# Kernel optimization log

Hardware: AMD Instinct MI355X
Metric: run time of the kernel (lower is better)

The kernel has to match this reference:

```python
import jax, jax.numpy as jnp
import numpy as np

BN_EPS = 1e-5


def conv3x3(x, w, b):
    # x: [B,C,H,W], w: [O,C,3,3], same padding, stride 1
    y = jax.lax.conv_general_dilated(x, w, (1, 1), ((1, 1), (1, 1)),
                                     dimension_numbers=('NCHW', 'OIHW', 'NCHW'))
    return y + b[None, :, None, None]


def bilinear_sample(x, py, px):
    # x: [B,C,H,W]; py/px: [B,K,H,W] fractional sample coords (zero outside borders)
    B, C, H, W = x.shape
    y0 = jnp.floor(py)
    x0 = jnp.floor(px)
    wy1 = py - y0  # frac weights
    wx1 = px - x0

    def corner(yc, xc, wgt):
        valid = (yc >= 0) & (yc <= H - 1) & (xc >= 0) & (xc <= W - 1)
        yi = jnp.clip(yc, 0, H - 1).astype(jnp.int32)
        xi = jnp.clip(xc, 0, W - 1).astype(jnp.int32)
        # gather per batch: [C,H,W] indexed by [K,H,W] -> [C,K,H,W]
        g = jax.vmap(lambda img, yy, xx: img[:, yy, xx])(x, yi, xi)  # [B,C,K,H,W]
        return g * jnp.where(valid, wgt, 0.0)[:, None]

    return (corner(y0, x0, (1 - wy1) * (1 - wx1))
            + corner(y0, x0 + 1, (1 - wy1) * wx1)
            + corner(y0 + 1, x0, wy1 * (1 - wx1))
            + corner(y0 + 1, x0 + 1, wy1 * wx1))  # [B,C,9,H,W]


def deform_conv(x, conv_w, off_w, off_b, mask_w, mask_b, gamma, beta):
    B, C, H, W = x.shape
    O = conv_w.shape[0]
    offset = conv3x3(x, off_w, off_b)                      # [B,18,H,W]
    mask = jax.nn.sigmoid(conv3x3(x, mask_w, mask_b))      # [B,9,H,W]
    off = offset.reshape(B, 9, 2, H, W)                    # tap k = kh*3+kw, (dy,dx)
    ky = jnp.repeat(jnp.arange(3), 3).astype(x.dtype)      # kernel row per tap
    kx = jnp.tile(jnp.arange(3), 3).astype(x.dtype)        # kernel col per tap
    gy = jnp.arange(H, dtype=x.dtype)
    gx = jnp.arange(W, dtype=x.dtype)
    # sample position = out pos - pad + kernel idx + learned offset
    py = off[:, :, 0] + gy[None, None, :, None] + (ky - 1.0)[None, :, None, None]
    px = off[:, :, 1] + gx[None, None, None, :] + (kx - 1.0)[None, :, None, None]
    val = bilinear_sample(x, py, px)                       # [B,C,9,H,W]
    val = val * mask[:, None]                              # modulated (DCNv2)
    out = jnp.einsum('bckhw,ock->bohw', val, conv_w.reshape(O, C, 9))
    # BatchNorm (training-mode batch stats) + ReLU
    mean = out.mean(axis=(0, 2, 3))
    var = out.var(axis=(0, 2, 3))
    out = (out - mean[None, :, None, None]) * jax.lax.rsqrt(var + BN_EPS)[None, :, None, None]
    out = out * gamma[None, :, None, None] + beta[None, :, None, None]
    return jax.nn.relu(out)


def setup_inputs() -> dict:
    key = jax.random.key(0)
    ks = jax.random.split(key, 8)
    B, Cin, Cout, H, W = 2, 64, 64, 128, 128
    x = jax.random.normal(ks[0], (B, Cin, H, W), dtype=jnp.float32)
    fan = Cin * 9
    conv_w = jax.random.normal(ks[1], (Cout, Cin, 3, 3), dtype=jnp.float32) / np.sqrt(fan)
    # offset/mask convs: small random weights so offsets are non-degenerate but modest
    off_w = jax.random.normal(ks[2], (18, Cin, 3, 3), dtype=jnp.float32) * 0.01
    off_b = jax.random.normal(ks[3], (18,), dtype=jnp.float32) * 0.1
    mask_w = jax.random.normal(ks[4], (9, Cin, 3, 3), dtype=jnp.float32) * 0.01
    mask_b = jnp.zeros((9,), dtype=jnp.float32)
    gamma = jnp.ones((Cout,), dtype=jnp.float32)
    beta = jnp.zeros((Cout,), dtype=jnp.float32)
    return {"x": x, "conv_w": conv_w, "off_w": off_w, "off_b": off_b,
            "mask_w": mask_w, "mask_b": mask_b, "gamma": gamma, "beta": beta}


def reference(x, conv_w, off_w, off_b, mask_w, mask_b, gamma, beta):
    return deform_conv(x, conv_w, off_w, off_b, mask_w, mask_b, gamma, beta)
```

## Files before the change

kernel.cpp:

```cpp
#include <hip/hip_runtime.h>
#include <hip/hip_fp16.h>

typedef __attribute__((ext_vector_type(8))) _Float16 f16x8;
typedef __attribute__((ext_vector_type(4))) float f32x4;
typedef __attribute__((ext_vector_type(4))) unsigned int u32x4;
typedef unsigned int  u32;
typedef unsigned short u16;

constexpr int B_  = 2;
constexpr int C_  = 64;
constexpr int O_  = 64;
constexpr int H_  = 128;
constexpr int W_  = 128;
constexpr int HW_ = H_ * W_;
constexpr int NPIX_ = B_ * HW_;
constexpr float BN_EPS_ = 1e-5f;

constexpr int WCOLS_ = 38;
constexpr int WPIX_  = 7 * WCOLS_;

__device__ __forceinline__ u16 f2bf(float f) {
    u32 u = __float_as_uint(f);
    u = (u + 0x7fffu + ((u >> 16) & 1u)) >> 16;
    return (u16)u;
}
__device__ __forceinline__ float bflo(u32 u) { return __uint_as_float(u << 16); }
__device__ __forceinline__ float bfhi(u32 u) { return __uint_as_float(u & 0xffff0000u); }
__device__ __forceinline__ u16 f2h(float f) { return __half_as_ushort(__float2half(f)); }

__device__ __forceinline__ u32 swz(u32 wpx, u32 seg) {
    return wpx * 64u + ((seg ^ (wpx & 7u)) * 8u);
}

__global__ __launch_bounds__(256)
void prep_kernel(const float* __restrict__ x, const float* __restrict__ conv_w,
                 const float* __restrict__ off_w, const float* __restrict__ mask_w,
                 u16* __restrict__ xt, u16* __restrict__ WpF, u16* __restrict__ W27F) {
    int bid = blockIdx.x, tid = threadIdx.x;
    if (bid < 512) {
        __shared__ u16 tile[64][66];
        int b = bid >> 8;
        int hw0 = (bid & 255) * 64;
        int c = tid >> 2, pq = (tid & 3) * 16;
        const float* src = x + (((size_t)(b * 64 + c)) << 14) + hw0 + pq;
#pragma unroll
        for (int i = 0; i < 4; i++) {
            float4 v = *(const float4*)(src + i * 4);
            tile[pq + i * 4 + 0][c] = f2h(v.x);
            tile[pq + i * 4 + 1][c] = f2h(v.y);
            tile[pq + i * 4 + 2][c] = f2h(v.z);
            tile[pq + i * 4 + 3][c] = f2h(v.w);
        }
        __syncthreads();
        int p = tid >> 2, cs = (tid & 3) * 16;
        uint4* dst = (uint4*)(xt + (((size_t)(b << 14)) + hw0 + p) * 64 + cs);
        dst[0] = *(const uint4*)&tile[p][cs];
        dst[1] = *(const uint4*)&tile[p][cs + 8];
    } else if (bid < 512 + 144) {
        int i = (bid - 512) * 256 + tid;
        int j = i & 7, lane = (i >> 3) & 63, t = (i >> 9) & 3, s = i >> 11;
        int o = t * 16 + (lane & 15);
        int kk = s * 32 + (lane >> 4) * 8 + j;
        int tap = kk >> 6, c = kk & 63;
        WpF[i] = f2h(conv_w[(o * 64 + c) * 9 + tap]);
    } else {
        int i = (bid - 656) * 256 + tid;
        int j = i & 7, lane = (i >> 3) & 63, t = (i >> 9) & 1, s = i >> 10;
        int row = t * 16 + (lane & 15);
        int kk = s * 32 + (lane >> 4) * 8 + j;
        int tap = kk >> 6, c = kk & 63;
        float v = 0.f;
        if (row < 18) v = off_w[(row * 64 + c) * 9 + tap];
        else if (row < 27) v = mask_w[((row - 18) * 64 + c) * 9 + tap];
        W27F[i] = f2h(v);
    }
}

__device__ __forceinline__ void metaBrt(const float* __restrict__ moff,
                                        const float* __restrict__ mmask,
                                        int tap, int p32, int h, int w, int cb,
                                        u32 quad, u32* qc, u32* cwp) {
    float dy = moff[(2 * tap) * 32 + p32];
    float dx = moff[(2 * tap + 1) * 32 + p32];
    float m  = mmask[tap * 32 + p32];
    float kdy = (float)(tap / 3 - 1), kdx = (float)(tap % 3 - 1);
    float py = dy + (float)h + kdy;
    float px = dx + (float)w + kdx;
    float y0 = floorf(py), x0 = floorf(px);
    float ly = py - y0, lx = px - x0, hy = 1.f - ly, hx = 1.f - lx;
    float y1 = y0 + 1.f, x1 = x0 + 1.f;
    bool vy0 = (y0 >= 0.f) && (y0 <= 127.f);
    bool vy1 = (y1 >= 0.f) && (y1 <= 127.f);
    bool vx0 = (x0 >= 0.f) && (x0 <= 127.f);
    bool vx1 = (x1 >= 0.f) && (x1 <= 127.f);
    int iy0 = (int)fminf(fmaxf(y0, 0.f), 127.f);
    int iy1 = (int)fminf(fmaxf(y1, 0.f), 127.f);
    int ix0 = (int)fminf(fmaxf(x0, 0.f), 127.f);
    int ix1 = (int)fminf(fmaxf(x1, 0.f), 127.f);
    int w00 = min(max(iy0 * WCOLS_ + ix0 - cb, 0), WPIX_ - 1);
    int w01 = min(max(iy0 * WCOLS_ + ix1 - cb, 0), WPIX_ - 1);
    int w10 = min(max(iy1 * WCOLS_ + ix0 - cb, 0), WPIX_ - 1);
    int w11 = min(max(iy1 * WCOLS_ + ix1 - cb, 0), WPIX_ - 1);
    qc[0] = swz((u32)w00, quad);
    qc[1] = swz((u32)w01, quad);
    qc[2] = swz((u32)w10, quad);
    qc[3] = swz((u32)w11, quad);
    __half2 c0 = __float2half2_rn((vy0 && vx0) ? hy * hx * m : 0.f);
    __half2 c1 = __float2half2_rn((vy0 && vx1) ? hy * lx * m : 0.f);
    __half2 c2 = __float2half2_rn((vy1 && vx0) ? ly * hx * m : 0.f);
    __half2 c3 = __float2half2_rn((vy1 && vx1) ? ly * lx * m : 0.f);
    cwp[0] = *(const u32*)&c0; cwp[1] = *(const u32*)&c1;
    cwp[2] = *(const u32*)&c2; cwp[3] = *(const u32*)&c3;
}

__device__ __forceinline__ void ld4x(const u16* __restrict__ win, const u32* qc,
                                     u32 sx, uint4* p) {
#pragma unroll
    for (int i = 0; i < 4; i++) p[i] = *(const uint4*)(win + (qc[i] ^ sx));
}

__device__ __forceinline__ f16x8 cmbH(const uint4* p, const u32* cwp) {
    const u32* a = &p[0].x; const u32* b = &p[1].x;
    const u32* c = &p[2].x; const u32* d = &p[3].x;
    __half2 cw0 = *(const __half2*)&cwp[0], cw1 = *(const __half2*)&cwp[1];
    __half2 cw2 = *(const __half2*)&cwp[2], cw3 = *(const __half2*)&cwp[3];
    u32x4 r;
#pragma unroll
    for (int i = 0; i < 4; i++) {
        __half2 t = __hmul2(*(const __half2*)&a[i], cw0);
        t = __hfma2(*(const __half2*)&b[i], cw1, t);
        t = __hfma2(*(const __half2*)&c[i], cw2, t);
        t = __hfma2(*(const __half2*)&d[i], cw3, t);
        r[i] = *(const u32*)&t;
    }
    return __builtin_bit_cast(f16x8, r);
}

template<int TAP>
__device__ __forceinline__ void tapB(const u16* __restrict__ win,
                                     const float* __restrict__ moff,
                                     const float* __restrict__ mmask,
                                     const u16* __restrict__ WpFo,
                                     int p32, int h, int w, int cb, u32 quad,
                                     int lane, uint4 (&pA)[4], u32 (&q)[4],
                                     u32 (&cw)[4], f32x4 (&acc)[2]) {
    uint4 pB[4];
    ld4x(win, q, 32, pB);
    u32 qn[4]; u32 wn[4]; uint4 pC[4];
    if constexpr (TAP < 8) {
        metaBrt(moff, mmask, TAP + 1, p32, h, w, cb, quad, qn, wn);
        ld4x(win, qn, 0, pC);
    }
    f16x8 sv = cmbH(pA, cw);
#pragma unroll
    for (int t = 0; t < 2; t++) {
        f16x8 af = *(const f16x8*)(WpFo + (u32)(2 * TAP) * 2048u + (u32)t * 512u + (u32)lane * 8u);
        acc[t] = __builtin_amdgcn_mfma_f32_16x16x32_f16(af, sv, acc[t], 0, 0, 0);
    }
    sv = cmbH(pB, cw);
#pragma unroll
    for (int t = 0; t < 2; t++) {
        f16x8 af = *(const f16x8*)(WpFo + (u32)(2 * TAP + 1) * 2048u + (u32)t * 512u + (u32)lane * 8u);
        acc[t] = __builtin_amdgcn_mfma_f32_16x16x32_f16(af, sv, acc[t], 0, 0, 0);
    }
    if constexpr (TAP < 8)
        tapB<TAP + 1>(win, moff, mmask, WpFo, p32, h, w, cb, quad, lane, pC, qn, wn, acc);
}

__global__ __launch_bounds__(256, 4)
void gemm_ab_kernel(const u16* __restrict__ xt, const u16* __restrict__ W27F,
                    const u16* __restrict__ WpF,
                    const float* __restrict__ off_b, const float* __restrict__ mask_b,
                    u16* __restrict__ pre16, float* __restrict__ part) {
    __shared__ __align__(16) u16 win[(WPIX_ + 1) * 64];
    __shared__ float moff[18 * 32];
    __shared__ float mmask[9 * 32];
    const int tid = threadIdx.x;
    const int lane = tid & 63, wv = tid >> 6;
    const int pxg = wv & 1, oh = wv >> 1;
    const u32 quad = (u32)(lane >> 4);
    const int r = lane & 15;
    const int pbase = blockIdx.x * 32;
    const int b = pbase >> 14, hwb = pbase & (HW_ - 1);
    const int h = hwb >> 7, w0 = hwb & (W_ - 1);
    const int p32 = pxg * 16 + r;
    const int hw = hwb + p32, w = w0 + p32;
    const int cb = (h - 3) * WCOLS_ + (w0 - 3);
    const u32 bb = (u32)b << 14;

#pragma unroll
    for (int it = 0; it < 9; it++) {
        int i = tid + it * 256;
        if (i < WPIX_ * 8) {
            u32 px = (u32)i >> 3, seg = (u32)i & 7u;
            int wr = (int)px / WCOLS_, wc = (int)px - wr * WCOLS_;
            int row = min(max(h - 3 + wr, 0), H_ - 1);
            int col = min(max(w0 - 3 + wc, 0), W_ - 1);
            u32 g = (bb + (u32)(row * W_ + col)) * 64u + seg * 8u;
            *(uint4*)(&win[swz(px, seg)]) = *(const uint4*)(xt + g);
        } else if (i < WPIX_ * 8 + 8) {
            u32 seg = (u32)(i - WPIX_ * 8);
            *(uint4*)(&win[swz((u32)WPIX_, seg)]) = make_uint4(0, 0, 0, 0);
        }
    }
    __syncthreads();

    {
        u32 aq[9];
#pragma unroll
        for (int tap = 0; tap < 9; tap++) {
            int dh = tap / 3 - 1, dw = tap % 3 - 1;
            int hh = h + dh, ww = w + dw;
            bool valid = (hh >= 0) && (hh < H_) && (ww >= 0) && (ww < W_);
            u32 wpx = valid ? (u32)((3 + dh) * WCOLS_ + (p32 + 3 + dw)) : (u32)WPIX_;
            aq[tap] = swz(wpx, quad);
        }
        const u16* W27Fo = W27F + (u32)oh * 512u;
        f32x4 accA = (f32x4){0.f, 0.f, 0.f, 0.f};
        f16x8 ab[3];
        ab[0] = *(const f16x8*)(win + aq[0]);
        ab[1] = *(const f16x8*)(win + (aq[0] ^ 32u));
        ab[2] = *(const f16x8*)(win + aq[1]);
#pragma unroll
        for (int s = 0; s < 18; s++) {
            f16x8 sv = ab[s % 3];
            if (s + 3 < 18)
                ab[s % 3] = *(const f16x8*)(win + (aq[(s + 3) >> 1] ^ (u32)(((s + 3) & 1) * 32)));
            f16x8 af = *(const f16x8*)(W27Fo + (u32)s * 1024u + (u32)lane * 8u);
            accA = __builtin_amdgcn_mfma_f32_16x16x32_f16(af, sv, accA, 0, 0, 0);
        }
#pragma unroll
        for (int g = 0; g < 4; g++) {
            int o = oh * 16 + (int)quad * 4 + g;
            float v = accA[g];
            if (o < 18) {
                moff[o * 32 + p32] = v + off_b[o];
            } else if (o < 27) {
                v += mask_b[o - 18];
                mmask[(o - 18) * 32 + p32] = 1.f / (1.f + __expf(-v));
            }
        }
    }
    __syncthreads();

    f32x4 acc[2];
    acc[0] = (f32x4){0.f, 0.f, 0.f, 0.f};
    acc[1] = (f32x4){0.f, 0.f, 0.f, 0.f};
    {
        const u16* WpFo = WpF + (u32)oh * 1024u;
        u32 q[4]; u32 cw[4];
        metaBrt(moff, mmask, 0, p32, h, w, cb, quad, q, cw);
        uint4 pA[4];
        ld4x(win, q, 0, pA);
        tapB<0>(win, moff, mmask, WpFo, p32, h, w, cb, quad, lane, pA, q, cw, acc);
    }

    const u32 slot = (u32)(blockIdx.x * 2 + pxg);
#pragma unroll
    for (int t = 0; t < 2; t++) {
#pragma unroll
        for (int g = 0; g < 4; g++) {
            float v = acc[t][g];
            int o = oh * 32 + t * 16 + (int)quad * 4 + g;
            pre16[(u32)(b * 64 + o) * HW_ + hw] = f2bf(v);
            float s = v, s2 = v * v;
#pragma unroll
            for (int off = 8; off >= 1; off >>= 1) {
                s  += __shfl_down(s, off, 16);
                s2 += __shfl_down(s2, off, 16);
            }
            if (r == 0) {
                part[(u32)o * 2048 + slot] = s;
                part[131072 + (u32)o * 2048 + slot] = s2;
            }
        }
    }
}

__global__ __launch_bounds__(256)
void stats_red_kernel(const float* __restrict__ part, float* __restrict__ stats) {
    __shared__ float p4[4];
    int i = blockIdx.x;
    const float* src = part + (u32)(i >> 6) * 131072 + (u32)(i & 63) * 2048;
    float s = 0.f;
    for (int rr = threadIdx.x; rr < 2048; rr += 256) s += src[rr];
#pragma unroll
    for (int off = 32; off >= 1; off >>= 1) s += __shfl_down(s, off);
    if ((threadIdx.x & 63) == 0) p4[threadIdx.x >> 6] = s;
    __syncthreads();
    if (threadIdx.x == 0) stats[i] = p4[0] + p4[1] + p4[2] + p4[3];
}

__global__ __launch_bounds__(256)
void bn_relu_kernel(const u16* __restrict__ pre16, const float* __restrict__ stats,
                    const float* __restrict__ gamma, const float* __restrict__ beta,
                    float* __restrict__ out) {
    int i4 = blockIdx.x * 256 + threadIdx.x;
    int ch = (i4 >> 12) & (O_ - 1);
    float mean = stats[ch] * (1.f / NPIX_);
    float var  = stats[64 + ch] * (1.f / NPIX_) - mean * mean;
    float scale = gamma[ch] * rsqrtf(var + BN_EPS_);
    float shift = beta[ch] - mean * scale;
    uint2 v = ((const uint2*)pre16)[i4];
    float4 o;
    o.x = fmaxf(fmaf(bflo(v.x), scale, shift), 0.f);
    o.y = fmaxf(fmaf(bfhi(v.x), scale, shift), 0.f);
    o.z = fmaxf(fmaf(bflo(v.y), scale, shift), 0.f);
    o.w = fmaxf(fmaf(bfhi(v.y), scale, shift), 0.f);
    ((float4*)out)[i4] = o;
}

extern "C" void kernel_launch(void* const* d_in, const int* in_sizes, int n_in,
                              void* d_out, int out_size, void* d_ws, size_t ws_size,
                              hipStream_t stream) {
    const float* x      = (const float*)d_in[0];
    const float* conv_w = (const float*)d_in[1];
    const float* off_w  = (const float*)d_in[2];
    const float* off_b  = (const float*)d_in[3];
    const float* mask_w = (const float*)d_in[4];
    const float* mask_b = (const float*)d_in[5];
    const float* gamma  = (const float*)d_in[6];
    const float* beta   = (const float*)d_in[7];
    float* out = (float*)d_out;

    char* ws = (char*)d_ws;
    u16*  xt     = (u16*)(ws);
    u16*  pre16  = (u16*)(ws + 4194432);
    u16*  WpF    = (u16*)(ws + 8388736);
    u16*  W27F   = (u16*)(ws + 8462464);
    float* part  = (float*)(ws + 8499328);
    float* stats = (float*)(ws + 9547904);

    prep_kernel<<<728, 256, 0, stream>>>(x, conv_w, off_w, mask_w, xt, WpF, W27F);
    gemm_ab_kernel<<<NPIX_ / 32, 256, 0, stream>>>(xt, W27F, WpF, off_b, mask_b, pre16, part);
    stats_red_kernel<<<128, 256, 0, stream>>>(part, stats);
    bn_relu_kernel<<<2048, 256, 0, stream>>>(pre16, stats, gamma, beta, out);
}
```

Measured before the change: 102.0 us.

## Software-pipeline MFMA loops, batch window loads, move BN stats to separate reduction

```diff
diff --git a/kernel.cpp b/kernel.cpp
--- a/kernel.cpp
+++ b/kernel.cpp
@@ -27,10 +27,14 @@
 __device__ __forceinline__ float bflo(u32 u) { return __uint_as_float(u << 16); }
 __device__ __forceinline__ float bfhi(u32 u) { return __uint_as_float(u & 0xffff0000u); }
 __device__ __forceinline__ u16 f2h(float f) { return __half_as_ushort(__float2half(f)); }
+__device__ __forceinline__ __half2 u2h2(u32 v) { return __builtin_bit_cast(__half2, v); }
+__device__ __forceinline__ u32 h22u(__half2 v) { return __builtin_bit_cast(u32, v); }
 
 __device__ __forceinline__ u32 swz(u32 wpx, u32 seg) {
     return wpx * 64u + ((seg ^ (wpx & 7u)) * 8u);
 }
+
+#define PIN() asm volatile("" ::: "memory")
 
 __global__ __launch_bounds__(256)
 void prep_kernel(const float* __restrict__ x, const float* __restrict__ conv_w,
@@ -76,10 +80,38 @@
     }
 }
 
+struct P4 { uint4 a, b, c, d; };
+
+__device__ __forceinline__ P4 ld4x(const u16* __restrict__ win, u32x4 qc, u32 sx) {
+    P4 p;
+    p.a = *(const uint4*)(win + (qc.x ^ sx));
+    p.b = *(const uint4*)(win + (qc.y ^ sx));
+    p.c = *(const uint4*)(win + (qc.z ^ sx));
+    p.d = *(const uint4*)(win + (qc.w ^ sx));
+    return p;
+}
+
+__device__ __forceinline__ f16x8 cmbH(const P4& p, u32x4 cw) {
+    const u32* a = &p.a.x; const u32* b = &p.b.x;
+    const u32* c = &p.c.x; const u32* d = &p.d.x;
+    __half2 cw0 = u2h2(cw.x), cw1 = u2h2(cw.y);
+    __half2 cw2 = u2h2(cw.z), cw3 = u2h2(cw.w);
+    u32x4 r;
+#pragma unroll
+    for (int i = 0; i < 4; i++) {
+        __half2 t = __hmul2(u2h2(a[i]), cw0);
+        t = __hfma2(u2h2(b[i]), cw1, t);
+        t = __hfma2(u2h2(c[i]), cw2, t);
+        t = __hfma2(u2h2(d[i]), cw3, t);
+        r[i] = h22u(t);
+    }
+    return __builtin_bit_cast(f16x8, r);
+}
+
 __device__ __forceinline__ void metaBrt(const float* __restrict__ moff,
                                         const float* __restrict__ mmask,
                                         int tap, int p32, int h, int w, int cb,
-                                        u32 quad, u32* qc, u32* cwp) {
+                                        u32 quad, u32x4& qc, u32x4& cw) {
     float dy = moff[(2 * tap) * 32 + p32];
     float dx = moff[(2 * tap + 1) * 32 + p32];
     float m  = mmask[tap * 32 + p32];
@@ -101,77 +133,66 @@
     int w01 = min(max(iy0 * WCOLS_ + ix1 - cb, 0), WPIX_ - 1);
     int w10 = min(max(iy1 * WCOLS_ + ix0 - cb, 0), WPIX_ - 1);
     int w11 = min(max(iy1 * WCOLS_ + ix1 - cb, 0), WPIX_ - 1);
-    qc[0] = swz((u32)w00, quad);
-    qc[1] = swz((u32)w01, quad);
-    qc[2] = swz((u32)w10, quad);
-    qc[3] = swz((u32)w11, quad);
-    __half2 c0 = __float2half2_rn((vy0 && vx0) ? hy * hx * m : 0.f);
-    __half2 c1 = __float2half2_rn((vy0 && vx1) ? hy * lx * m : 0.f);
-    __half2 c2 = __float2half2_rn((vy1 && vx0) ? ly * hx * m : 0.f);
-    __half2 c3 = __float2half2_rn((vy1 && vx1) ? ly * lx * m : 0.f);
-    cwp[0] = *(const u32*)&c0; cwp[1] = *(const u32*)&c1;
-    cwp[2] = *(const u32*)&c2; cwp[3] = *(const u32*)&c3;
-}
-
-__device__ __forceinline__ void ld4x(const u16* __restrict__ win, const u32* qc,
-                                     u32 sx, uint4* p) {
-#pragma unroll
-    for (int i = 0; i < 4; i++) p[i] = *(const uint4*)(win + (qc[i] ^ sx));
-}
-
-__device__ __forceinline__ f16x8 cmbH(const uint4* p, const u32* cwp) {
-    const u32* a = &p[0].x; const u32* b = &p[1].x;
-    const u32* c = &p[2].x; const u32* d = &p[3].x;
-    __half2 cw0 = *(const __half2*)&cwp[0], cw1 = *(const __half2*)&cwp[1];
-    __half2 cw2 = *(const __half2*)&cwp[2], cw3 = *(const __half2*)&cwp[3];
-    u32x4 r;
-#pragma unroll
-    for (int i = 0; i < 4; i++) {
-        __half2 t = __hmul2(*(const __half2*)&a[i], cw0);
-        t = __hfma2(*(const __half2*)&b[i], cw1, t);
-        t = __hfma2(*(const __half2*)&c[i], cw2, t);
-        t = __hfma2(*(const __half2*)&d[i], cw3, t);
-        r[i] = *(const u32*)&t;
-    }
-    return __builtin_bit_cast(f16x8, r);
-}
-
-template<int TAP>
-__device__ __forceinline__ void tapB(const u16* __restrict__ win,
-                                     const float* __restrict__ moff,
-                                     const float* __restrict__ mmask,
-                                     const u16* __restrict__ WpFo,
-                                     int p32, int h, int w, int cb, u32 quad,
-                                     int lane, uint4 (&pA)[4], u32 (&q)[4],
-                                     u32 (&cw)[4], f32x4 (&acc)[2]) {
-    uint4 pB[4];
-    ld4x(win, q, 32, pB);
-    u32 qn[4]; u32 wn[4]; uint4 pC[4];
-    if constexpr (TAP < 8) {
-        metaBrt(moff, mmask, TAP + 1, p32, h, w, cb, quad, qn, wn);
-        ld4x(win, qn, 0, pC);
-    }
-    f16x8 sv = cmbH(pA, cw);
-#pragma unroll
-    for (int t = 0; t < 2; t++) {
-        f16x8 af = *(const f16x8*)(WpFo + (u32)(2 * TAP) * 2048u + (u32)t * 512u + (u32)lane * 8u);
-        acc[t] = __builtin_amdgcn_mfma_f32_16x16x32_f16(af, sv, acc[t], 0, 0, 0);
-    }
-    sv = cmbH(pB, cw);
-#pragma unroll
-    for (int t = 0; t < 2; t++) {
-        f16x8 af = *(const f16x8*)(WpFo + (u32)(2 * TAP + 1) * 2048u + (u32)t * 512u + (u32)lane * 8u);
-        acc[t] = __builtin_amdgcn_mfma_f32_16x16x32_f16(af, sv, acc[t], 0, 0, 0);
-    }
-    if constexpr (TAP < 8)
-        tapB<TAP + 1>(win, moff, mmask, WpFo, p32, h, w, cb, quad, lane, pC, qn, wn, acc);
-}
-
-__global__ __launch_bounds__(256, 4)
+    qc.x = swz((u32)w00, quad);
+    qc.y = swz((u32)w01, quad);
+    qc.z = swz((u32)w10, quad);
+    qc.w = swz((u32)w11, quad);
+    cw.x = h22u(__float2half2_rn((vy0 && vx0) ? hy * hx * m : 0.f));
+    cw.y = h22u(__float2half2_rn((vy0 && vx1) ? hy * lx * m : 0.f));
+    cw.z = h22u(__float2half2_rn((vy1 && vx0) ? ly * hx * m : 0.f));
+    cw.w = h22u(__float2half2_rn((vy1 && vx1) ? ly * lx * m : 0.f));
+}
+
+template<int S>
+__device__ __forceinline__ void stepA(const u16* __restrict__ win,
+                                      const u16* __restrict__ W27Fo, int lane,
+                                      const u32 (&aq)[9], f16x8 sCur, f16x8 aCur,
+                                      f32x4& accA) {
+    f16x8 sN{}, aN{};
+    if constexpr (S + 1 < 18) {
+        sN = *(const f16x8*)(win + (aq[(S + 1) >> 1] ^ (u32)(((S + 1) & 1) * 32)));
+        aN = *(const f16x8*)(W27Fo + (u32)(S + 1) * 1024u + (u32)lane * 8u);
+    }
+    PIN();
+    accA = __builtin_amdgcn_mfma_f32_16x16x32_f16(aCur, sCur, accA, 0, 0, 0);
+    if constexpr (S + 1 < 18)
+        stepA<S + 1>(win, W27Fo, lane, aq, sN, aN, accA);
+}
+
+template<int S>
+__device__ __forceinline__ void stepB(const u16* __restrict__ win,
+                                      const float* __restrict__ moff,
+                                      const float* __restrict__ mmask,
+                                      const u16* __restrict__ WpFo,
+                                      int p32, int h, int w, int cb, u32 quad,
+                                      int lane, P4 pCur, f16x8 a0, f16x8 a1,
+                                      u32x4 q, u32x4 cw, f32x4 (&acc)[2]) {
+    P4 pN{}; f16x8 n0{}, n1{};
+    u32x4 qn = q, wn = cw;
+    if constexpr (S + 1 < 18) {
+        if constexpr (((S + 1) & 1) == 0) {
+            metaBrt(moff, mmask, (S + 1) >> 1, p32, h, w, cb, quad, qn, wn);
+            pN = ld4x(win, qn, 0);
+        } else {
+            pN = ld4x(win, q, 32);
+        }
+        n0 = *(const f16x8*)(WpFo + (u32)(S + 1) * 2048u + (u32)lane * 8u);
+        n1 = *(const f16x8*)(WpFo + (u32)(S + 1) * 2048u + 512u + (u32)lane * 8u);
+    }
+    PIN();
+    f16x8 sv = cmbH(pCur, cw);
+    acc[0] = __builtin_amdgcn_mfma_f32_16x16x32_f16(a0, sv, acc[0], 0, 0, 0);
+    acc[1] = __builtin_amdgcn_mfma_f32_16x16x32_f16(a1, sv, acc[1], 0, 0, 0);
+    if constexpr (S + 1 < 18)
+        stepB<S + 1>(win, moff, mmask, WpFo, p32, h, w, cb, quad, lane,
+                     pN, n0, n1, qn, wn, acc);
+}
+
+__global__ __launch_bounds__(256, 3)
 void gemm_ab_kernel(const u16* __restrict__ xt, const u16* __restrict__ W27F,
                     const u16* __restrict__ WpF,
                     const float* __restrict__ off_b, const float* __restrict__ mask_b,
-                    u16* __restrict__ pre16, float* __restrict__ part) {
+                    u16* __restrict__ pre16) {
     __shared__ __align__(16) u16 win[(WPIX_ + 1) * 64];
     __shared__ float moff[18 * 32];
     __shared__ float mmask[9 * 32];
@@ -188,19 +209,30 @@
     const int cb = (h - 3) * WCOLS_ + (w0 - 3);
     const u32 bb = (u32)b << 14;
 
-#pragma unroll
-    for (int it = 0; it < 9; it++) {
-        int i = tid + it * 256;
-        if (i < WPIX_ * 8) {
-            u32 px = (u32)i >> 3, seg = (u32)i & 7u;
-            int wr = (int)px / WCOLS_, wc = (int)px - wr * WCOLS_;
-            int row = min(max(h - 3 + wr, 0), H_ - 1);
-            int col = min(max(w0 - 3 + wc, 0), W_ - 1);
-            u32 g = (bb + (u32)(row * W_ + col)) * 64u + seg * 8u;
-            *(uint4*)(&win[swz(px, seg)]) = *(const uint4*)(xt + g);
-        } else if (i < WPIX_ * 8 + 8) {
-            u32 seg = (u32)(i - WPIX_ * 8);
-            *(uint4*)(&win[swz((u32)WPIX_, seg)]) = make_uint4(0, 0, 0, 0);
+    {
+        uint4 ldv[9];
+#pragma unroll
+        for (int it = 0; it < 9; it++) {
+            int i = tid + it * 256;
+            uint4 v = make_uint4(0, 0, 0, 0);
+            if (i < WPIX_ * 8) {
+                u32 px = (u32)i >> 3, seg = (u32)i & 7u;
+                int wr = (int)(px / (u32)WCOLS_), wc = (int)px - wr * WCOLS_;
+                int row = min(max(h - 3 + wr, 0), H_ - 1);
+                int col = min(max(w0 - 3 + wc, 0), W_ - 1);
+                u32 g = (bb + (u32)(row * W_ + col)) * 64u + seg * 8u;
+                v = *(const uint4*)(xt + g);
+            }
+            ldv[it] = v;
+        }
+        PIN();
+#pragma unroll
+        for (int it = 0; it < 9; it++) {
+            int i = tid + it * 256;
+            if (i < WPIX_ * 8 + 8) {
+                u32 px = (u32)i >> 3, seg = (u32)i & 7u;
+                *(uint4*)(&win[swz(px, seg)]) = ldv[it];
+            }
         }
     }
     __syncthreads();
@@ -217,18 +249,9 @@
         }
         const u16* W27Fo = W27F + (u32)oh * 512u;
         f32x4 accA = (f32x4){0.f, 0.f, 0.f, 0.f};
-        f16x8 ab[3];
-        ab[0] = *(const f16x8*)(win + aq[0]);
-        ab[1] = *(const f16x8*)(win + (aq[0] ^ 32u));
-        ab[2] = *(const f16x8*)(win + aq[1]);
-#pragma unroll
-        for (int s = 0; s < 18; s++) {
-            f16x8 sv = ab[s % 3];
-            if (s + 3 < 18)
-                ab[s % 3] = *(const f16x8*)(win + (aq[(s + 3) >> 1] ^ (u32)(((s + 3) & 1) * 32)));
-            f16x8 af = *(const f16x8*)(W27Fo + (u32)s * 1024u + (u32)lane * 8u);
-            accA = __builtin_amdgcn_mfma_f32_16x16x32_f16(af, sv, accA, 0, 0, 0);
-        }
+        f16x8 s0 = *(const f16x8*)(win + aq[0]);
+        f16x8 a0 = *(const f16x8*)(W27Fo + (u32)lane * 8u);
+        stepA<0>(win, W27Fo, lane, aq, s0, a0, accA);
 #pragma unroll
         for (int g = 0; g < 4; g++) {
             int o = oh * 16 + (int)quad * 4 + g;
@@ -248,47 +271,56 @@
     acc[1] = (f32x4){0.f, 0.f, 0.f, 0.f};
     {
         const u16* WpFo = WpF + (u32)oh * 1024u;
-        u32 q[4]; u32 cw[4];
-        metaBrt(moff, mmask, 0, p32, h, w, cb, quad, q, cw);
-        uint4 pA[4];
-        ld4x(win, q, 0, pA);
-        tapB<0>(win, moff, mmask, WpFo, p32, h, w, cb, quad, lane, pA, q, cw, acc);
-    }
-
-    const u32 slot = (u32)(blockIdx.x * 2 + pxg);
+        u32x4 q0, w0c;
+        metaBrt(moff, mmask, 0, p32, h, w, cb, quad, q0, w0c);
+        P4 p0 = ld4x(win, q0, 0);
+        f16x8 b0 = *(const f16x8*)(WpFo + (u32)lane * 8u);
+        f16x8 b1 = *(const f16x8*)(WpFo + 512u + (u32)lane * 8u);
+        stepB<0>(win, moff, mmask, WpFo, p32, h, w, cb, quad, lane,
+                 p0, b0, b1, q0, w0c, acc);
+    }
+
 #pragma unroll
     for (int t = 0; t < 2; t++) {
 #pragma unroll
         for (int g = 0; g < 4; g++) {
-            float v = acc[t][g];
             int o = oh * 32 + t * 16 + (int)quad * 4 + g;
-            pre16[(u32)(b * 64 + o) * HW_ + hw] = f2bf(v);
-            float s = v, s2 = v * v;
-#pragma unroll
-            for (int off = 8; off >= 1; off >>= 1) {
-                s  += __shfl_down(s, off, 16);
-                s2 += __shfl_down(s2, off, 16);
+            pre16[(u32)(b * 64 + o) * HW_ + hw] = f2bf(acc[t][g]);
+        }
+    }
+}
+
+__global__ __launch_bounds__(256)
+void stats_red_kernel(const u16* __restrict__ pre16, float* __restrict__ stats) {
+    __shared__ float p8[8];
+    int ch = blockIdx.x;
+    int tid = threadIdx.x;
+    float s = 0.f, s2 = 0.f;
+#pragma unroll
+    for (int b2 = 0; b2 < 2; b2++) {
+        const u16* src = pre16 + ((u32)(b2 * 64 + ch) << 14);
+        for (int i = tid * 8; i < HW_; i += 2048) {
+            uint4 v = *(const uint4*)(src + i);
+            const u32* pv = &v.x;
+#pragma unroll
+            for (int k = 0; k < 4; k++) {
+                float lo = bflo(pv[k]), hi = bfhi(pv[k]);
+                s += lo + hi;
+                s2 += lo * lo + hi * hi;
             }
-            if (r == 0) {
-                part[(u32)o * 2048 + slot] = s;
-                part[131072 + (u32)o * 2048 + slot] = s2;
-            }
-        }
-    }
-}
-
-__global__ __launch_bounds__(256)
-void stats_red_kernel(const float* __restrict__ part, float* __restrict__ stats) {
-    __shared__ float p4[4];
-    int i = blockIdx.x;
-    const float* src = part + (u32)(i >> 6) * 131072 + (u32)(i & 63) * 2048;
-    float s = 0.f;
-    for (int rr = threadIdx.x; rr < 2048; rr += 256) s += src[rr];
-#pragma unroll
-    for (int off = 32; off >= 1; off >>= 1) s += __shfl_down(s, off);
-    if ((threadIdx.x & 63) == 0) p4[threadIdx.x >> 6] = s;
+        }
+    }
+#pragma unroll
+    for (int off = 32; off >= 1; off >>= 1) {
+        s  += __shfl_down(s, off);
+        s2 += __shfl_down(s2, off);
+    }
+    if ((tid & 63) == 0) { p8[tid >> 6] = s; p8[4 + (tid >> 6)] = s2; }
     __syncthreads();
-    if (threadIdx.x == 0) stats[i] = p4[0] + p4[1] + p4[2] + p4[3];
+    if (tid == 0) {
+        stats[ch]      = p8[0] + p8[1] + p8[2] + p8[3];
+        stats[64 + ch] = p8[4] + p8[5] + p8[6] + p8[7];
+    }
 }
 
 __global__ __launch_bounds__(256)
@@ -328,11 +360,10 @@
     u16*  pre16  = (u16*)(ws + 4194432);
     u16*  WpF    = (u16*)(ws + 8388736);
     u16*  W27F   = (u16*)(ws + 8462464);
-    float* part  = (float*)(ws + 8499328);
     float* stats = (float*)(ws + 9547904);
 
     prep_kernel<<<728, 256, 0, stream>>>(x, conv_w, off_w, mask_w, xt, WpF, W27F);
-    gemm_ab_kernel<<<NPIX_ / 32, 256, 0, stream>>>(xt, W27F, WpF, off_b, mask_b, pre16, part);
-    stats_red_kernel<<<128, 256, 0, stream>>>(part, stats);
+    gemm_ab_kernel<<<NPIX_ / 32, 256, 0, stream>>>(xt, W27F, WpF, off_b, mask_b, pre16);
+    stats_red_kernel<<<64, 256, 0, stream>>>(pre16, stats);
     bn_relu_kernel<<<2048, 256, 0, stream>>>(pre16, stats, gamma, beta, out);
 }
```

Measured after the change: 103.4 us. No clear change (+1.4%).
